# Kernel tuning notes

Measured on AMD Instinct MI355X. Metric: run time of the kernel, lower is better.

The kernel has to match this reference:

```python
import jax, jax.numpy as jnp
import numpy as np

NEG_SLOPE = 0.2  # PyG GATConv default leaky_relu slope
N_NODES, N_EDGES, F_IN, HID = 25000, 200000, 64, 128


def gat_layer(x, src, dst, W, a_src, a_dst, b, heads, ch):
    """PyG-style GATConv (concat=True, eval mode). x:[N,Fin] -> [N,heads*ch]."""
    N = x.shape[0]
    h = (x @ W).reshape(N, heads, ch)                      # [N,H,C]
    al_s = jnp.sum(h * a_src, axis=-1)                     # [N,H]
    al_d = jnp.sum(h * a_dst, axis=-1)                     # [N,H]
    e = jax.nn.leaky_relu(al_s[src] + al_d[dst], NEG_SLOPE)  # [E,H]
    # segment softmax over incoming edges of each dst node (stable)
    e = e - jax.ops.segment_max(e, dst, num_segments=N)[dst]
    ex = jnp.exp(e)
    alpha = ex / jax.ops.segment_sum(ex, dst, num_segments=N)[dst]  # [E,H]
    out = jax.ops.segment_sum(h[src] * alpha[:, :, None], dst, num_segments=N)  # [N,H,C]
    return out.reshape(N, heads * ch) + b


def setup_inputs() -> dict:
    key = jax.random.key(0)
    ks = jax.random.split(key, 24)
    def g(k, shape, fan_in):
        return jax.random.normal(k, shape, dtype=jnp.float32) / np.sqrt(fan_in)
    inp = {
        "x": jax.random.normal(ks[0], (N_NODES, F_IN), dtype=jnp.float32),
        "edge_index": jax.random.randint(ks[1], (2, N_EDGES), 0, N_NODES, dtype=jnp.int64) if jax.config.jax_enable_x64 else jax.random.randint(ks[1], (2, N_EDGES), 0, N_NODES).astype(jnp.int32),
        "liquor_idx": jax.random.randint(ks[2], (4096,), 0, N_NODES),
        "ingredient_idx": jax.random.randint(ks[3], (4096,), 0, N_NODES),
        "W1": g(ks[4], (F_IN, 8 * HID), F_IN), "a_s1": g(ks[5], (8, HID), HID), "a_d1": g(ks[6], (8, HID), HID), "b1": jnp.zeros((8 * HID,), jnp.float32),
        "W2": g(ks[7], (8 * HID, 8 * HID), 8 * HID), "a_s2": g(ks[8], (8, HID), HID), "a_d2": g(ks[9], (8, HID), HID), "b2": jnp.zeros((8 * HID,), jnp.float32),
        "W3": g(ks[10], (8 * HID, HID), 8 * HID), "a_s3": g(ks[11], (1, HID), HID), "a_d3": g(ks[12], (1, HID), HID), "b3": jnp.zeros((HID,), jnp.float32),
        # MLP scorer: 256 -> 128 -> 64 -> 1
        "mw1": g(ks[13], (2 * HID, HID), 2 * HID), "mb1": jnp.zeros((HID,), jnp.float32),
        "mw2": g(ks[14], (HID, HID // 2), HID), "mb2": jnp.zeros((HID // 2,), jnp.float32),
        "mw3": g(ks[15], (HID // 2, 1), HID // 2), "mb3": jnp.zeros((1,), jnp.float32),
    }
    return inp


def reference(x, edge_index, liquor_idx, ingredient_idx,
              W1, a_s1, a_d1, b1, W2, a_s2, a_d2, b2, W3, a_s3, a_d3, b3,
              mw1, mb1, mw2, mb2, mw3, mb3):
    N = x.shape[0]
    loops = jnp.arange(N, dtype=edge_index.dtype)  # GATConv adds self-loops
    src = jnp.concatenate([edge_index[0], loops])
    dst = jnp.concatenate([edge_index[1], loops])
    h = jax.nn.relu(gat_layer(x, src, dst, W1, a_s1, a_d1, b1, 8, HID))
    h = jax.nn.relu(gat_layer(h, src, dst, W2, a_s2, a_d2, b2, 8, HID))
    h = gat_layer(h, src, dst, W3, a_s3, a_d3, b3, 1, HID)
    pair = jnp.concatenate([h[liquor_idx], h[ingredient_idx]], axis=-1)  # [B,256]
    z = jax.nn.relu(pair @ mw1 + mb1)
    z = jax.nn.relu(z @ mw2 + mb2)
    z = z @ mw3 + mb3
    return jax.nn.sigmoid(z).squeeze(-1)
```

## Files before the change

### kernel.cpp

```cpp
#include <hip/hip_runtime.h>
#include <math.h>

#define NEG_SLOPE 0.2f

typedef short short8 __attribute__((ext_vector_type(8)));
typedef float f32x4 __attribute__((ext_vector_type(4)));

__device__ __forceinline__ float lrelu(float x){ return x > 0.f ? x : NEG_SLOPE * x; }

__device__ __forceinline__ unsigned short f2bf(float f){
  union { float f; unsigned u; } v; v.f = f;
  unsigned r = v.u + 0x7fff + ((v.u >> 16) & 1);
  return (unsigned short)(r >> 16);
}
__device__ __forceinline__ float bf2f(unsigned short u){
  union { unsigned u; float f; } v; v.u = ((unsigned)u) << 16; return v.f;
}

__device__ __forceinline__ void gld16(const unsigned short* g, unsigned short* l){
  __builtin_amdgcn_global_load_lds(
      (const __attribute__((address_space(1))) unsigned int*)g,
      (__attribute__((address_space(3))) unsigned int*)l, 16, 0, 0);
}

__global__ void k_count(const int* __restrict__ dst, int* __restrict__ cnt, int E){
  int e = blockIdx.x*blockDim.x + threadIdx.x;
  if (e < E) atomicAdd(&cnt[dst[e]], 1);
}

__global__ void k_blockscan(const int* __restrict__ cnt, int* __restrict__ row,
                            int* __restrict__ aux, int n){
  __shared__ int buf[256];
  int t = threadIdx.x;
  int base = blockIdx.x * 256;
  int v = (base + t < n) ? cnt[base + t] : 0;
  buf[t] = v;
  __syncthreads();
  #pragma unroll
  for (int off = 1; off < 256; off <<= 1){
    int u = (t >= off) ? buf[t - off] : 0;
    __syncthreads();
    buf[t] += u;
    __syncthreads();
  }
  if (base + t < n) row[base + t + 1] = buf[t];
  if (t == 255) aux[blockIdx.x] = buf[255];
  if (blockIdx.x == 0 && t == 0) row[0] = 0;
}

__global__ void k_addoff(const int* __restrict__ aux, int* __restrict__ row, int n){
  __shared__ int s_pre;
  int b = blockIdx.x, t = threadIdx.x;
  if (t == 0){
    int pre = 0;
    for (int i = 0; i < b; ++i) pre += aux[i];
    s_pre = pre;
  }
  __syncthreads();
  int i = b * 256 + t;
  if (i < n) row[i + 1] += s_pre;
}

__global__ void k_scatter(const int* __restrict__ src, const int* __restrict__ dst,
                          const int* __restrict__ row, int* __restrict__ cur,
                          int* __restrict__ csr, int E){
  int e = blockIdx.x*blockDim.x + threadIdx.x;
  if (e < E){
    int d = dst[e];
    int p = atomicAdd(&cur[d], 1);
    csr[row[d] + p] = src[e];
  }
}

__global__ void k_prep(const float* __restrict__ x, unsigned short* __restrict__ xb, int nx, int nxb,
                       const float* __restrict__ W1, unsigned short* __restrict__ Wt1,
                       const float* __restrict__ W2, unsigned short* __restrict__ Wt2,
                       const float* __restrict__ W3, unsigned short* __restrict__ Wt3){
  __shared__ float tile[32][33];
  int b = blockIdx.x, t = threadIdx.x;
  if (b < nxb){
    int i0 = b * 2048 + t * 8;
    if (i0 + 8 <= nx){
      float4 f0 = *reinterpret_cast<const float4*>(x + i0);
      float4 f1 = *reinterpret_cast<const float4*>(x + i0 + 4);
      short8 o;
      o[0]=f2bf(f0.x); o[1]=f2bf(f0.y); o[2]=f2bf(f0.z); o[3]=f2bf(f0.w);
      o[4]=f2bf(f1.x); o[5]=f2bf(f1.y); o[6]=f2bf(f1.z); o[7]=f2bf(f1.w);
      *reinterpret_cast<short8*>(xb + i0) = o;
    } else {
      for (int k = 0; k < 8 && i0 + k < nx; ++k) xb[i0 + k] = f2bf(x[i0 + k]);
    }
    return;
  }
  const float* W; unsigned short* Wt; int K, N, ti;
  if (b < nxb + 64)            { W = W1; Wt = Wt1; K = 64;   N = 1024; ti = b - nxb;
                                 int kb = (ti & 1) * 32, nb = (ti >> 1) * 32;
                                 int tx = t & 31, ty = t >> 5;
                                 #pragma unroll
                                 for (int i = ty; i < 32; i += 8) tile[i][tx] = W[(size_t)(kb+i)*N + nb+tx];
                                 __syncthreads();
                                 #pragma unroll
                                 for (int i = ty; i < 32; i += 8) Wt[(size_t)(nb+i)*K + kb+tx] = f2bf(tile[tx][i]);
                                 return; }
  if (b < nxb + 64 + 1024)     { W = W2; Wt = Wt2; K = 1024; N = 1024; ti = b - nxb - 64; }
  else                         { W = W3; Wt = Wt3; K = 1024; N = 128;  ti = b - nxb - 64 - 1024; }
  int kb = (ti & 31) * 32, nb = (ti >> 5) * 32;
  int tx = t & 31, ty = t >> 5;
  #pragma unroll
  for (int i = ty; i < 32; i += 8) tile[i][tx] = W[(size_t)(kb+i)*N + nb+tx];
  __syncthreads();
  #pragma unroll
  for (int i = ty; i < 32; i += 8) Wt[(size_t)(nb+i)*K + kb+tx] = f2bf(tile[tx][i]);
}

template<int HEADS>
__global__ __launch_bounds__(256) void k_gemm_fused(
    const unsigned short* __restrict__ A,
    const unsigned short* __restrict__ Bt,
    unsigned short* __restrict__ C,
    const float* __restrict__ a_s, const float* __restrict__ a_d,
    float* __restrict__ ALS, float* __restrict__ ALD,
    int M, int N, int K, int gxc){
  __shared__ unsigned short SMEM[2 * 128 * 32];
  unsigned short* As = SMEM;
  unsigned short* Bs = SMEM + 128 * 32;
  const int nwg = gridDim.x;
  int bid = blockIdx.x;
  int swz = ((nwg & 7) == 0) ? ((bid & 7) * (nwg >> 3) + (bid >> 3)) : bid;
  const int bxi = swz % gxc, byi = swz / gxc;
  const int bm = byi * 128, bn = bxi * 128;
  const int head = bxi;
  const int tid  = threadIdx.x;
  const int lane = tid & 63, wave = tid >> 6;
  const int wr = wave >> 1, wc = wave & 1;
  const int lr = lane & 15, lk = lane >> 4;
  const int srow = wave * 16 + (lane >> 2);
  const int skc  = (lane & 3) * 8;
  int ar0 = bm + srow;      if (ar0 >= M) ar0 = M - 1;
  int ar1 = bm + srow + 64; if (ar1 >= M) ar1 = M - 1;
  const unsigned short* ga0 = A  + (size_t)ar0 * K + skc;
  const unsigned short* ga1 = A  + (size_t)ar1 * K + skc;
  const unsigned short* gb0 = Bt + (size_t)(bn + srow) * K + skc;
  const unsigned short* gb1 = Bt + (size_t)(bn + srow + 64) * K + skc;
  f32x4 acc[4][4] = {};
  for (int k0 = 0; k0 < K; k0 += 32){
    gld16(ga0 + k0, &As[(size_t)wave * 512]);
    gld16(ga1 + k0, &As[(size_t)(wave + 4) * 512]);
    gld16(gb0 + k0, &Bs[(size_t)wave * 512]);
    gld16(gb1 + k0, &Bs[(size_t)(wave + 4) * 512]);
    __syncthreads();
    short8 af[4], bg[4];
    #pragma unroll
    for (int m = 0; m < 4; ++m)
      af[m] = *reinterpret_cast<const short8*>(&As[(wr * 64 + m * 16 + lr) * 32 + lk * 8]);
    #pragma unroll
    for (int n = 0; n < 4; ++n)
      bg[n] = *reinterpret_cast<const short8*>(&Bs[(wc * 64 + n * 16 + lr) * 32 + lk * 8]);
    #pragma unroll
    for (int m = 0; m < 4; ++m)
      #pragma unroll
      for (int n = 0; n < 4; ++n)
        acc[m][n] = __builtin_amdgcn_mfma_f32_16x16x32_bf16(af[m], bg[n], acc[m][n], 0, 0, 0);
    __syncthreads();
  }
  #pragma unroll
  for (int m = 0; m < 4; ++m){
    #pragma unroll
    for (int j = 0; j < 4; ++j){
      int rowi = bm + wr * 64 + m * 16 + lk * 4 + j;
      if (rowi < M){
        #pragma unroll
        for (int n = 0; n < 4; ++n)
          C[(size_t)rowi * N + bn + wc * 64 + n * 16 + lr] = f2bf(acc[m][n][j]);
      }
    }
  }
  float as4[4], ad4[4];
  #pragma unroll
  for (int n = 0; n < 4; ++n){
    as4[n] = a_s[head * 128 + wc * 64 + n * 16 + lr];
    ad4[n] = a_d[head * 128 + wc * 64 + n * 16 + lr];
  }
  float* red = (float*)SMEM;
  #pragma unroll
  for (int m = 0; m < 4; ++m){
    #pragma unroll
    for (int j = 0; j < 4; ++j){
      float ps = 0.f;
      #pragma unroll
      for (int n = 0; n < 4; ++n) ps = fmaf(acc[m][n][j], as4[n], ps);
      red[(wr * 64 + m * 16 + lk * 4 + j) * 32 + wc * 16 + lr] = ps;
    }
  }
  __syncthreads();
  if (tid < 128){
    float s = 0.f;
    #pragma unroll
    for (int i = 0; i < 32; ++i) s += red[tid * 32 + ((i + tid) & 31)];
    int gr = bm + tid;
    if (gr < M) ALS[(size_t)gr * HEADS + head] = s;
  }
  __syncthreads();
  #pragma unroll
  for (int m = 0; m < 4; ++m){
    #pragma unroll
    for (int j = 0; j < 4; ++j){
      float pd = 0.f;
      #pragma unroll
      for (int n = 0; n < 4; ++n) pd = fmaf(acc[m][n][j], ad4[n], pd);
      red[(wr * 64 + m * 16 + lk * 4 + j) * 32 + wc * 16 + lr] = pd;
    }
  }
  __syncthreads();
  if (tid < 128){
    float s = 0.f;
    #pragma unroll
    for (int i = 0; i < 32; ++i) s += red[tid * 32 + ((i + tid) & 31)];
    int gr = bm + tid;
    if (gr < M) ALD[(size_t)gr * HEADS + head] = s;
  }
}

__global__ __launch_bounds__(512, 2) void k_gemm256(
    const unsigned short* __restrict__ A,
    const unsigned short* __restrict__ Bt,
    unsigned short* __restrict__ C,
    const float* __restrict__ a_s, const float* __restrict__ a_d,
    float* __restrict__ ALS, float* __restrict__ ALD,
    int M, int N, int K, int gxc){
  __shared__ unsigned short smem[2 * 24576];
  const int nwg = gridDim.x;
  int bid = blockIdx.x;
  int swz = ((nwg & 7) == 0) ? ((bid & 7) * (nwg >> 3) + (bid >> 3)) : bid;
  const int bxi = swz % gxc, byi = swz / gxc;
  const int bm = byi * 256, bn = bxi * 128, head = bxi;
  const int tid = threadIdx.x;
  const int lane = tid & 63, wave = tid >> 6;
  const int wr = wave >> 1, wc = wave & 1;
  const int lr = lane & 15, lk = lane >> 4;
  const int sr   = tid >> 3;
  const int scol = ((tid & 7) << 3) ^ ((sr & 7) << 3);
  size_t offA[4], offB[2];
  #pragma unroll
  for (int u = 0; u < 4; ++u){
    int r = bm + u * 64 + sr; if (r >= M) r = M - 1;
    offA[u] = (size_t)r * K + scol;
  }
  #pragma unroll
  for (int u = 0; u < 2; ++u)
    offB[u] = (size_t)(bn + u * 64 + sr) * K + scol;
  const int wdst = (tid >> 6) * 512;

  f32x4 acc[4][4] = {};
  short8 af[4][2], bg[4][2];
  const int NKT = K >> 6;
  const int rsw = (lr & 7) << 3;

  #pragma unroll
  for (int u = 0; u < 4; ++u) gld16(A + offA[u], &smem[u * 4096 + wdst]);
  #pragma unroll
  for (int u = 0; u < 2; ++u) gld16(Bt + offB[u], &smem[16384 + u * 4096 + wdst]);
  #pragma unroll
  for (int u = 0; u < 4; ++u) gld16(A + offA[u] + 64, &smem[24576 + u * 4096 + wdst]);
  asm volatile("s_waitcnt vmcnt(4)" ::: "memory");
  __builtin_amdgcn_s_barrier();

  for (int kt = 0; kt < NKT; ++kt){
    const int s = kt & 1;
    const unsigned short* sa = &smem[s * 24576];
    const unsigned short* sb = &smem[s * 24576 + 16384];
    #pragma unroll
    for (int m = 0; m < 4; ++m){
      int r = (wr * 64 + m * 16 + lr) * 64;
      af[m][0] = *reinterpret_cast<const short8*>(&sa[r + ((lk * 8) ^ rsw)]);
      af[m][1] = *reinterpret_cast<const short8*>(&sa[r + ((32 + lk * 8) ^ rsw)]);
    }
    #pragma unroll
    for (int n = 0; n < 2; ++n){
      int r = (wc * 64 + n * 16 + lr) * 64;
      bg[n][0] = *reinterpret_cast<const short8*>(&sb[r + ((lk * 8) ^ rsw)]);
      bg[n][1] = *reinterpret_cast<const short8*>(&sb[r + ((32 + lk * 8) ^ rsw)]);
    }
    if (kt + 1 < NKT){
      int so = (s ^ 1) * 24576 + 16384;
      gld16(Bt + offB[0] + (size_t)(kt + 1) * 64, &smem[so + wdst]);
      gld16(Bt + offB[1] + (size_t)(kt + 1) * 64, &smem[so + 4096 + wdst]);
    }
    __builtin_amdgcn_s_barrier();
    asm volatile("s_waitcnt lgkmcnt(0)" ::: "memory");
    __builtin_amdgcn_sched_barrier(0);
    __builtin_amdgcn_s_setprio(1);
    #pragma unroll
    for (int m = 0; m < 4; ++m)
      #pragma unroll
      for (int n = 0; n < 2; ++n){
        acc[m][n] = __builtin_amdgcn_mfma_f32_16x16x32_bf16(af[m][0], bg[n][0], acc[m][n], 0, 0, 0);
        acc[m][n] = __builtin_amdgcn_mfma_f32_16x16x32_bf16(af[m][1], bg[n][1], acc[m][n], 0, 0, 0);
      }
    __builtin_amdgcn_s_setprio(0);
    __builtin_amdgcn_s_barrier();
    #pragma unroll
    for (int n = 2; n < 4; ++n){
      int r = (wc * 64 + n * 16 + lr) * 64;
      bg[n][0] = *reinterpret_cast<const short8*>(&sb[r + ((lk * 8) ^ rsw)]);
      bg[n][1] = *reinterpret_cast<const short8*>(&sb[r + ((32 + lk * 8) ^ rsw)]);
    }
    if (kt + 2 < NKT){
      int so = s * 24576;
      #pragma unroll
      for (int u = 0; u < 4; ++u)
        gld16(A + offA[u] + (size_t)(kt + 2) * 64, &smem[so + u * 4096 + wdst]);
    }
    __builtin_amdgcn_s_barrier();
    asm volatile("s_waitcnt lgkmcnt(0)" ::: "memory");
    __builtin_amdgcn_sched_barrier(0);
    __builtin_amdgcn_s_setprio(1);
    #pragma unroll
    for (int m = 0; m < 4; ++m)
      #pragma unroll
      for (int n = 2; n < 4; ++n){
        acc[m][n] = __builtin_amdgcn_mfma_f32_16x16x32_bf16(af[m][0], bg[n][0], acc[m][n], 0, 0, 0);
        acc[m][n] = __builtin_amdgcn_mfma_f32_16x16x32_bf16(af[m][1], bg[n][1], acc[m][n], 0, 0, 0);
      }
    __builtin_amdgcn_s_setprio(0);
    asm volatile("s_waitcnt vmcnt(4)" ::: "memory");
    __builtin_amdgcn_s_barrier();
  }

  #pragma unroll
  for (int m = 0; m < 4; ++m)
    #pragma unroll
    for (int j = 0; j < 4; ++j){
      int row = bm + wr * 64 + m * 16 + lk * 4 + j;
      if (row < M){
        #pragma unroll
        for (int n = 0; n < 4; ++n)
          C[(size_t)row * N + bn + wc * 64 + n * 16 + lr] = f2bf(acc[m][n][j]);
      }
    }
  float as4[4], ad4[4];
  #pragma unroll
  for (int n = 0; n < 4; ++n){
    as4[n] = a_s[head * 128 + wc * 64 + n * 16 + lr];
    ad4[n] = a_d[head * 128 + wc * 64 + n * 16 + lr];
  }
  asm volatile("s_waitcnt vmcnt(0)" ::: "memory");
  __builtin_amdgcn_s_barrier();
  float2* red = (float2*)smem;
  #pragma unroll
  for (int m = 0; m < 4; ++m)
    #pragma unroll
    for (int j = 0; j < 4; ++j){
      float ps = 0.f, pd = 0.f;
      #pragma unroll
      for (int n = 0; n < 4; ++n){
        ps = fmaf(acc[m][n][j], as4[n], ps);
        pd = fmaf(acc[m][n][j], ad4[n], pd);
      }
      red[(wr * 64 + m * 16 + lk * 4 + j) * 32 + wc * 16 + lr] = make_float2(ps, pd);
    }
  __syncthreads();
  if (tid < 256){
    float ss = 0.f, sd = 0.f;
    #pragma unroll
    for (int i = 0; i < 32; ++i){
      float2 v = red[tid * 32 + ((i + tid) & 31)];
      ss += v.x; sd += v.y;
    }
    int gr = bm + tid;
    if (gr < M){
      ALS[(size_t)gr * 8 + head] = ss;
      ALD[(size_t)gr * 8 + head] = sd;
    }
  }
}

template<int HEADS, int VEC, int OUTBF>
__global__ void k_gat_bf(const unsigned short* __restrict__ hp, const float* __restrict__ al_s,
                         const float* __restrict__ al_d, const int* __restrict__ row,
                         const int* __restrict__ csr, const float* __restrict__ bias,
                         void* __restrict__ outv, int N, int do_relu){
  constexpr int TPH = 128 / VEC;
  int n = blockIdx.x;
  int t = threadIdx.x;
  int h = t / TPH;
  int c0 = (t % TPH) * VEC;
  float ald = al_d[(size_t)n * HEADS + h];
  float mA = lrelu(al_s[(size_t)n * HEADS + h] + ald);
  float lA = 1.f;
  float accA[VEC], accB[VEC];
  float mB = -1e30f, lB = 0.f;
  const unsigned short* hpn = hp + ((size_t)n * HEADS + h) * 128 + c0;
  if constexpr (VEC == 8){
    short8 hv8 = *reinterpret_cast<const short8*>(hpn);
    #pragma unroll
    for (int v = 0; v < 8; ++v){ accA[v] = bf2f((unsigned short)hv8[v]); accB[v] = 0.f; }
  } else {
    ushort2 hv2 = *reinterpret_cast<const ushort2*>(hpn);
    accA[0] = bf2f(hv2.x); accA[1] = bf2f(hv2.y);
    accB[0] = 0.f; accB[1] = 0.f;
  }
  int beg = row[n], end = row[n + 1];
  int j = beg;
  for (; j + 1 < end; j += 2){
    int s0 = csr[j], s1 = csr[j + 1];
    float e0 = lrelu(al_s[(size_t)s0 * HEADS + h] + ald);
    float e1 = lrelu(al_s[(size_t)s1 * HEADS + h] + ald);
    const unsigned short* p0 = hp + ((size_t)s0 * HEADS + h) * 128 + c0;
    const unsigned short* p1 = hp + ((size_t)s1 * HEADS + h) * 128 + c0;
    if constexpr (VEC == 8){
      short8 v0 = *reinterpret_cast<const short8*>(p0);
      short8 v1 = *reinterpret_cast<const short8*>(p1);
      float mn0 = fmaxf(mA, e0), mn1 = fmaxf(mB, e1);
      float sc0 = __expf(mA - mn0), sc1 = __expf(mB - mn1);
      float pw0 = __expf(e0 - mn0), pw1 = __expf(e1 - mn1);
      #pragma unroll
      for (int v = 0; v < 8; ++v){
        accA[v] = accA[v] * sc0 + pw0 * bf2f((unsigned short)v0[v]);
        accB[v] = accB[v] * sc1 + pw1 * bf2f((unsigned short)v1[v]);
      }
      lA = lA * sc0 + pw0; mA = mn0;
      lB = lB * sc1 + pw1; mB = mn1;
    } else {
      ushort2 v0 = *reinterpret_cast<const ushort2*>(p0);
      ushort2 v1 = *reinterpret_cast<const ushort2*>(p1);
      float mn0 = fmaxf(mA, e0), mn1 = fmaxf(mB, e1);
      float sc0 = __expf(mA - mn0), sc1 = __expf(mB - mn1);
      float pw0 = __expf(e0 - mn0), pw1 = __expf(e1 - mn1);
      accA[0] = accA[0] * sc0 + pw0 * bf2f(v0.x);
      accA[1] = accA[1] * sc0 + pw0 * bf2f(v0.y);
      accB[0] = accB[0] * sc1 + pw1 * bf2f(v1.x);
      accB[1] = accB[1] * sc1 + pw1 * bf2f(v1.y);
      lA = lA * sc0 + pw0; mA = mn0;
      lB = lB * sc1 + pw1; mB = mn1;
    }
  }
  if (j < end){
    int s0 = csr[j];
    float e0 = lrelu(al_s[(size_t)s0 * HEADS + h] + ald);
    const unsigned short* p0 = hp + ((size_t)s0 * HEADS + h) * 128 + c0;
    float mn0 = fmaxf(mA, e0);
    float sc0 = __expf(mA - mn0), pw0 = __expf(e0 - mn0);
    if constexpr (VEC == 8){
      short8 v0 = *reinterpret_cast<const short8*>(p0);
      #pragma unroll
      for (int v = 0; v < 8; ++v) accA[v] = accA[v] * sc0 + pw0 * bf2f((unsigned short)v0[v]);
    } else {
      ushort2 v0 = *reinterpret_cast<const ushort2*>(p0);
      accA[0] = accA[0] * sc0 + pw0 * bf2f(v0.x);
      accA[1] = accA[1] * sc0 + pw0 * bf2f(v0.y);
    }
    lA = lA * sc0 + pw0; mA = mn0;
  }
  float mn = fmaxf(mA, mB);
  float sA = __expf(mA - mn), sB = __expf(mB - mn);
  float l = lA * sA + lB * sB;
  float inv = 1.f / l;
  size_t ob = ((size_t)n * HEADS + h) * 128 + c0;
  #pragma unroll
  for (int v = 0; v < VEC; ++v){
    float o = (accA[v] * sA + accB[v] * sB) * inv + bias[h * 128 + c0 + v];
    if (do_relu) o = fmaxf(o, 0.f);
    if constexpr (OUTBF) ((unsigned short*)outv)[ob + v] = f2bf(o);
    else                 ((float*)outv)[ob + v] = o;
  }
}

__global__ void k_mlp(const float* __restrict__ h3, const int* __restrict__ liq,
                      const int* __restrict__ ing,
                      const float* __restrict__ mw1, const float* __restrict__ mb1,
                      const float* __restrict__ mw2, const float* __restrict__ mb2,
                      const float* __restrict__ mw3, const float* __restrict__ mb3,
                      float* __restrict__ out, int B){
  __shared__ float pairv[256];
  __shared__ float z1[128];
  __shared__ float z2[64];
  int r = blockIdx.x;
  int t = threadIdx.x;
  pairv[t]       = h3[(size_t)liq[r] * 128 + t];
  pairv[128 + t] = h3[(size_t)ing[r] * 128 + t];
  __syncthreads();
  float a1 = mb1[t];
  for (int k = 0; k < 256; ++k) a1 = fmaf(pairv[k], mw1[k * 128 + t], a1);
  z1[t] = fmaxf(a1, 0.f);
  __syncthreads();
  if (t < 64){
    float a2 = mb2[t];
    for (int k = 0; k < 128; ++k) a2 = fmaf(z1[k], mw2[k * 64 + t], a2);
    z2[t] = fmaxf(a2, 0.f);
  }
  __syncthreads();
  if (t < 64){
    float p = z2[t] * mw3[t];
    #pragma unroll
    for (int off = 32; off >= 1; off >>= 1) p += __shfl_xor(p, off);
    if (t == 0) out[r] = 1.f / (1.f + __expf(-(p + mb3[0])));
  }
}

extern "C" void kernel_launch(void* const* d_in, const int* in_sizes, int n_in,
                              void* d_out, int out_size, void* d_ws, size_t ws_size,
                              hipStream_t stream){
  const float* x   = (const float*)d_in[0];
  const int*   ei  = (const int*)  d_in[1];
  const int*   liq = (const int*)  d_in[2];
  const int*   ing = (const int*)  d_in[3];
  const float* W1  = (const float*)d_in[4];
  const float* as1 = (const float*)d_in[5];
  const float* ad1 = (const float*)d_in[6];
  const float* b1  = (const float*)d_in[7];
  const float* W2  = (const float*)d_in[8];
  const float* as2 = (const float*)d_in[9];
  const float* ad2 = (const float*)d_in[10];
  const float* b2  = (const float*)d_in[11];
  const float* W3  = (const float*)d_in[12];
  const float* as3 = (const float*)d_in[13];
  const float* ad3 = (const float*)d_in[14];
  const float* b3  = (const float*)d_in[15];
  const float* mw1 = (const float*)d_in[16];
  const float* mb1 = (const float*)d_in[17];
  const float* mw2 = (const float*)d_in[18];
  const float* mb2 = (const float*)d_in[19];
  const float* mw3 = (const float*)d_in[20];
  const float* mb3 = (const float*)d_in[21];
  float* out = (float*)d_out;

  const int N = in_sizes[0] / 64;
  const int E = in_sizes[1] / 2;
  const int B = in_sizes[2];
  const int* srcp = ei;
  const int* dstp = ei + E;

  char* w = (char*)d_ws;
  auto alloc = [&](size_t bytes) -> char* {
    char* p = w;
    w += (bytes + 255) & ~(size_t)255;
    return p;
  };
  unsigned short* P    = (unsigned short*)alloc((size_t)N * 1024 * 2);
  unsigned short* Hb   = (unsigned short*)alloc((size_t)N * 1024 * 2);
  float*          H3   = (float*)         alloc((size_t)N * 128 * 4);
  unsigned short* xb   = (unsigned short*)alloc((size_t)N * 64 * 2);
  unsigned short* Wt1  = (unsigned short*)alloc((size_t)1024 * 64 * 2);
  unsigned short* Wt2  = (unsigned short*)alloc((size_t)1024 * 1024 * 2);
  unsigned short* Wt3  = (unsigned short*)alloc((size_t)128 * 1024 * 2);
  float* ALS  = (float*)alloc((size_t)N * 8 * 4);
  float* ALD  = (float*)alloc((size_t)N * 8 * 4);
  int*   row  = (int*)  alloc((size_t)(N + 1) * 4);
  int*   cntcur = (int*)alloc((size_t)2 * N * 4);
  int*   cnt  = cntcur;
  int*   cur  = cntcur + N;
  int*   aux  = (int*)  alloc((size_t)256 * 4);
  int*   csr  = (int*)  alloc((size_t)E * 4);
  (void)ws_size; (void)n_in; (void)out_size;

  int nx = N * 64;
  int nxb = (nx + 2047) / 2048;
  k_prep<<<nxb + 64 + 1024 + 128, 256, 0, stream>>>(x, xb, nx, nxb, W1, Wt1, W2, Wt2, W3, Wt3);

  hipMemsetAsync(cntcur, 0, (size_t)2 * N * 4, stream);
  int eb = (E + 255) / 256;
  int nb = (N + 255) / 256;
  k_count<<<eb, 256, 0, stream>>>(dstp, cnt, E);
  k_blockscan<<<nb, 256, 0, stream>>>(cnt, row, aux, N);
  k_addoff<<<nb, 256, 0, stream>>>(aux, row, N);
  k_scatter<<<eb, 256, 0, stream>>>(srcp, dstp, row, cur, csr, E);

  const int mt  = (N + 127) / 128;
  const int mt2 = (N + 255) / 256;

  k_gemm_fused<8><<<8 * mt, 256, 0, stream>>>(xb, Wt1, P, as1, ad1, ALS, ALD, N, 1024, 64, 8);
  k_gat_bf<8,8,1><<<N, 128, 0, stream>>>(P, ALS, ALD, row, csr, b1, Hb, N, 1);

  k_gemm256<<<8 * mt2, 512, 0, stream>>>(Hb, Wt2, P, as2, ad2, ALS, ALD, N, 1024, 1024, 8);
  k_gat_bf<8,8,1><<<N, 128, 0, stream>>>(P, ALS, ALD, row, csr, b2, Hb, N, 1);

  k_gemm_fused<1><<<1 * mt, 256, 0, stream>>>(Hb, Wt3, P, as3, ad3, ALS, ALD, N, 128, 1024, 1);
  k_gat_bf<1,2,0><<<N, 64, 0, stream>>>(P, ALS, ALD, row, csr, b3, H3, N, 0);

  k_mlp<<<B, 128, 0, stream>>>(H3, liq, ing, mw1, mb1, mw2, mb2, mw3, mb3, out, B);
}
```

Before: 356.7 us.

## Reorder layer-1 GAT to aggregate raw inputs before projection

Layer 1 now aggregates the 64-dim input features per head before projecting, instead of projecting to 1024 dims and aggregating those. The attention logits are computed from x with precomputed W1·a_s and W1·a_d vectors. Per-head aggregated features (512 wide) then go through a per-head GEMM with bias and ReLU fused in. This cuts gather traffic in the layer-1 edge aggregation roughly eightfold, at the cost of three extra kernels and an online-softmax loop that recomputes exponentials per lane.

```diff
diff --git a/kernel.cpp b/kernel.cpp
--- a/kernel.cpp
+++ b/kernel.cpp
@@ -111,6 +111,152 @@
   __syncthreads();
   #pragma unroll
   for (int i = ty; i < 32; i += 8) Wt[(size_t)(nb+i)*K + kb+tx] = f2bf(tile[tx][i]);
+}
+
+__global__ void k_fold(const float* __restrict__ W1, const float* __restrict__ a_s,
+                       const float* __restrict__ a_d, float* __restrict__ ws){
+  int k = blockIdx.x, t = threadIdx.x;
+  int h = t >> 5, l = t & 31;
+  float4 wv = *reinterpret_cast<const float4*>(&W1[(size_t)k * 1024 + h * 128 + l * 4]);
+  float4 sv = *reinterpret_cast<const float4*>(&a_s[h * 128 + l * 4]);
+  float4 dv = *reinterpret_cast<const float4*>(&a_d[h * 128 + l * 4]);
+  float ps = wv.x*sv.x + wv.y*sv.y + wv.z*sv.z + wv.w*sv.w;
+  float pd = wv.x*dv.x + wv.y*dv.y + wv.z*dv.z + wv.w*dv.w;
+  #pragma unroll
+  for (int off = 16; off >= 1; off >>= 1){
+    ps += __shfl_xor(ps, off);
+    pd += __shfl_xor(pd, off);
+  }
+  if (l == 0){ ws[k * 16 + h] = ps; ws[k * 16 + 8 + h] = pd; }
+}
+
+__global__ void k_logits1(const unsigned short* __restrict__ xb, const float* __restrict__ ws,
+                          float* __restrict__ ALS, float* __restrict__ ALD, int N){
+  __shared__ unsigned short lx[32 * 64];
+  __shared__ float lw[64 * 16];
+  int t = threadIdx.x;
+  int n0 = blockIdx.x * 32;
+  int r = t >> 3, c = (t & 7) * 8;
+  if (n0 + r < N)
+    *reinterpret_cast<short8*>(&lx[r * 64 + c]) =
+      *reinterpret_cast<const short8*>(&xb[(size_t)(n0 + r) * 64 + c]);
+  else {
+    short8 z = {0,0,0,0,0,0,0,0};
+    *reinterpret_cast<short8*>(&lx[r * 64 + c]) = z;
+  }
+  *reinterpret_cast<float4*>(&lw[t * 4]) = *reinterpret_cast<const float4*>(&ws[t * 4]);
+  __syncthreads();
+  int nl = t >> 3, h = t & 7;
+  if (n0 + nl >= N) return;
+  float s = 0.f, d = 0.f;
+  #pragma unroll 8
+  for (int k = 0; k < 64; ++k){
+    float xv = bf2f(lx[nl * 64 + k]);
+    s = fmaf(xv, lw[k * 16 + h], s);
+    d = fmaf(xv, lw[k * 16 + 8 + h], d);
+  }
+  ALS[(size_t)(n0 + nl) * 8 + h] = s;
+  ALD[(size_t)(n0 + nl) * 8 + h] = d;
+}
+
+__global__ void k_gat_x(const unsigned short* __restrict__ xb, const float* __restrict__ ALS,
+                        const float* __restrict__ ALD, const int* __restrict__ row,
+                        const int* __restrict__ csr, unsigned short* __restrict__ G, int N){
+  int t = threadIdx.x;
+  int n = blockIdx.x * 4 + (t >> 6);
+  if (n >= N) return;
+  int lane = t & 63;
+  float ald[8], m[8], l[8], acc[8];
+  float xv = bf2f(xb[(size_t)n * 64 + lane]);
+  #pragma unroll
+  for (int h = 0; h < 8; ++h){
+    ald[h] = ALD[(size_t)n * 8 + h];
+    m[h] = lrelu(ALS[(size_t)n * 8 + h] + ald[h]);
+    l[h] = 1.f;
+    acc[h] = xv;
+  }
+  int beg = row[n], end = row[n + 1];
+  for (int j = beg; j < end; ++j){
+    int s = csr[j];
+    float xs = bf2f(xb[(size_t)s * 64 + lane]);
+    #pragma unroll
+    for (int h = 0; h < 8; ++h){
+      float e = lrelu(ALS[(size_t)s * 8 + h] + ald[h]);
+      float mn = fmaxf(m[h], e);
+      float sc = __expf(m[h] - mn);
+      float p  = __expf(e - mn);
+      acc[h] = acc[h] * sc + p * xs;
+      l[h]   = l[h] * sc + p;
+      m[h]   = mn;
+    }
+  }
+  #pragma unroll
+  for (int h = 0; h < 8; ++h)
+    G[(size_t)n * 512 + h * 64 + lane] = f2bf(acc[h] / l[h]);
+}
+
+__global__ __launch_bounds__(256) void k_gemm_g(
+    const unsigned short* __restrict__ G,
+    const unsigned short* __restrict__ Bt,
+    const float* __restrict__ bias,
+    unsigned short* __restrict__ C,
+    int M){
+  __shared__ unsigned short As[128 * 32];
+  __shared__ unsigned short Bs[128 * 32];
+  const int nwg = gridDim.x;
+  int bid = blockIdx.x;
+  int swz = ((nwg & 7) == 0) ? ((bid & 7) * (nwg >> 3) + (bid >> 3)) : bid;
+  const int head = swz % 8, byi = swz / 8;
+  const int bm = byi * 128, bn = head * 128;
+  const int tid  = threadIdx.x;
+  const int lane = tid & 63, wave = tid >> 6;
+  const int wr = wave >> 1, wc = wave & 1;
+  const int lr = lane & 15, lk = lane >> 4;
+  const int srow = wave * 16 + (lane >> 2);
+  const int skc  = (lane & 3) * 8;
+  int ar0 = bm + srow;      if (ar0 >= M) ar0 = M - 1;
+  int ar1 = bm + srow + 64; if (ar1 >= M) ar1 = M - 1;
+  const unsigned short* ga0 = G + (size_t)ar0 * 512 + head * 64 + skc;
+  const unsigned short* ga1 = G + (size_t)ar1 * 512 + head * 64 + skc;
+  const unsigned short* gb0 = Bt + (size_t)(bn + srow) * 64 + skc;
+  const unsigned short* gb1 = Bt + (size_t)(bn + srow + 64) * 64 + skc;
+  f32x4 acc[4][4] = {};
+  #pragma unroll
+  for (int k0 = 0; k0 < 64; k0 += 32){
+    gld16(ga0 + k0, &As[(size_t)wave * 512]);
+    gld16(ga1 + k0, &As[(size_t)(wave + 4) * 512]);
+    gld16(gb0 + k0, &Bs[(size_t)wave * 512]);
+    gld16(gb1 + k0, &Bs[(size_t)(wave + 4) * 512]);
+    __syncthreads();
+    short8 af[4], bg[4];
+    #pragma unroll
+    for (int m = 0; m < 4; ++m)
+      af[m] = *reinterpret_cast<const short8*>(&As[(wr * 64 + m * 16 + lr) * 32 + lk * 8]);
+    #pragma unroll
+    for (int n = 0; n < 4; ++n)
+      bg[n] = *reinterpret_cast<const short8*>(&Bs[(wc * 64 + n * 16 + lr) * 32 + lk * 8]);
+    #pragma unroll
+    for (int m = 0; m < 4; ++m)
+      #pragma unroll
+      for (int n = 0; n < 4; ++n)
+        acc[m][n] = __builtin_amdgcn_mfma_f32_16x16x32_bf16(af[m], bg[n], acc[m][n], 0, 0, 0);
+    __syncthreads();
+  }
+  float bv[4];
+  #pragma unroll
+  for (int n = 0; n < 4; ++n) bv[n] = bias[bn + wc * 64 + n * 16 + lr];
+  #pragma unroll
+  for (int m = 0; m < 4; ++m){
+    #pragma unroll
+    for (int j = 0; j < 4; ++j){
+      int rowi = bm + wr * 64 + m * 16 + lk * 4 + j;
+      if (rowi < M){
+        #pragma unroll
+        for (int n = 0; n < 4; ++n)
+          C[(size_t)rowi * 1024 + bn + wc * 64 + n * 16 + lr] = f2bf(fmaxf(acc[m][n][j] + bv[n], 0.f));
+      }
+    }
+  }
 }
 
 template<int HEADS>
@@ -546,17 +692,20 @@
   unsigned short* Wt3  = (unsigned short*)alloc((size_t)128 * 1024 * 2);
   float* ALS  = (float*)alloc((size_t)N * 8 * 4);
   float* ALD  = (float*)alloc((size_t)N * 8 * 4);
+  float* ws1  = (float*)alloc((size_t)64 * 16 * 4);
   int*   row  = (int*)  alloc((size_t)(N + 1) * 4);
   int*   cntcur = (int*)alloc((size_t)2 * N * 4);
   int*   cnt  = cntcur;
   int*   cur  = cntcur + N;
   int*   aux  = (int*)  alloc((size_t)256 * 4);
   int*   csr  = (int*)  alloc((size_t)E * 4);
+  unsigned short* G = P;
   (void)ws_size; (void)n_in; (void)out_size;
 
   int nx = N * 64;
   int nxb = (nx + 2047) / 2048;
   k_prep<<<nxb + 64 + 1024 + 128, 256, 0, stream>>>(x, xb, nx, nxb, W1, Wt1, W2, Wt2, W3, Wt3);
+  k_fold<<<64, 256, 0, stream>>>(W1, as1, ad1, ws1);
 
   hipMemsetAsync(cntcur, 0, (size_t)2 * N * 4, stream);
   int eb = (E + 255) / 256;
@@ -569,8 +718,9 @@
   const int mt  = (N + 127) / 128;
   const int mt2 = (N + 255) / 256;
 
-  k_gemm_fused<8><<<8 * mt, 256, 0, stream>>>(xb, Wt1, P, as1, ad1, ALS, ALD, N, 1024, 64, 8);
-  k_gat_bf<8,8,1><<<N, 128, 0, stream>>>(P, ALS, ALD, row, csr, b1, Hb, N, 1);
+  k_logits1<<<(N + 31) / 32, 256, 0, stream>>>(xb, ws1, ALS, ALD, N);
+  k_gat_x<<<(N + 3) / 4, 256, 0, stream>>>(xb, ALS, ALD, row, csr, G, N);
+  k_gemm_g<<<8 * mt, 256, 0, stream>>>(G, Wt1, b1, Hb, N);
 
   k_gemm256<<<8 * mt2, 512, 0, stream>>>(Hb, Wt2, P, as2, ad2, ALS, ALD, N, 1024, 1024, 8);
   k_gat_bf<8,8,1><<<N, 128, 0, stream>>>(P, ALS, ALD, row, csr, b2, Hb, N, 1);
```

New measurement: 353.7 us. Within noise of the previous version (-0.8%).
